# Kernel optimization log

Measured on AMD Instinct MI355X. Metric: run time of the kernel, lower is better.

## Reference

```python
import jax, jax.numpy as jnp
import numpy as np

B, D, H = 64, 2048, 2048


def setup_inputs() -> dict:
    key = jax.random.key(0)
    ks = jax.random.split(key, 10)
    s = 1.0 / np.sqrt(D)  # Linear init scale
    # small z scale keeps exp() gates in a sane range
    return {
        "t": jnp.zeros((), jnp.float32),
        "z": jax.random.normal(ks[0], (B, D), jnp.float32) * 0.02,
        "K": jax.random.normal(ks[1], (B, D), jnp.float32) * 0.02,
        "V": jax.random.normal(ks[2], (B, D, D), jnp.float32) * 0.02,
        "Wq": jax.random.normal(ks[3], (D, D), jnp.float32) * s,
        "bq": jnp.zeros((D,), jnp.float32),
        "Wk": jax.random.normal(ks[4], (D, D), jnp.float32) * s,
        "bk": jnp.zeros((D,), jnp.float32),
        "Wv": jax.random.normal(ks[5], (D, D), jnp.float32) * s,
        "bv": jnp.zeros((D,), jnp.float32),
        "W1": jax.random.normal(ks[6], (D, H), jnp.float32) * s,
        "b1": jnp.zeros((H,), jnp.float32),
        "W2": jax.random.normal(ks[7], (H, D), jnp.float32) * (1.0 / np.sqrt(H)),
        "b2": jnp.zeros((D,), jnp.float32),
    }


def reference(t, z, K, V, Wq, bq, Wk, bk, Wv, bv, W1, b1, W2, b2):
    # get_ode_gradient_nn: 2-layer tanh MLP (stand-in for user ode_func_net)
    dz = jnp.tanh(z @ W1 + b1) @ W2 + b2                 # [B, D]
    dK = jnp.exp(z @ Wk + bk)                            # exp gate, [B, D]
    v = z @ Wv + bv                                      # [B, D]
    dV = jnp.einsum("bd,be->bde", v, dK)                # rank-1 outer update, [B, D, D]
    q = jnp.exp(z @ Wq + bq)                             # [B, D]
    a = jnp.sum(q * dK, axis=-1, keepdims=True)          # q . dK, [B, 1]
    dq = q * (dz @ Wq + bq)                              # [B, D]
    da = a + jnp.sum(dq * K, axis=-1, keepdims=True)     # [B, 1]
    dc = jnp.einsum("bde,be->bd", dV, q) + jnp.einsum("bde,be->bd", V, dq)  # [B, D]
    return (dz, da, dc, dK, dV)
```

## Files before the change

### kernel.cpp

```cpp
#include <hip/hip_runtime.h>
#include <cstddef>
#include <math.h>

#define BB 64
#define DD 2048
#define HH 2048
#define BD (BB*DD)
#define WN (2048*2048)

typedef unsigned short u16;
typedef __attribute__((ext_vector_type(8))) short bf16x8;
typedef __attribute__((ext_vector_type(4))) float f32x4;
typedef __attribute__((ext_vector_type(4))) float f4;

__device__ __forceinline__ u16 f2b(float x) {
    union { float f; unsigned u; } v; v.f = x;
    unsigned r = v.u + 0x7FFFu + ((v.u >> 16) & 1u);
    return (u16)(r >> 16);
}

__device__ __forceinline__ void gload16(const void* g, void* l) {
    __builtin_amdgcn_global_load_lds(
        (__attribute__((address_space(1))) void*)g,
        (__attribute__((address_space(3))) void*)l, 16, 0, 0);
}


__device__ __forceinline__ void wconv_tile(
    u16* sm, const float* __restrict__ W, u16* __restrict__ T,
    int kb, int nb)
{
    int t = threadIdx.x;
    int k0 = kb * 64, n0 = nb * 64;
    {
        int r = t >> 2, c0 = (t & 3) * 16;
        const float* src = W + (size_t)(k0 + r) * DD + n0 + c0;
#pragma unroll
        for (int q = 0; q < 4; ++q) {
            float4 f = *(const float4*)(src + q * 4);
            sm[r * 66 + c0 + q*4 + 0] = f2b(f.x);
            sm[r * 66 + c0 + q*4 + 1] = f2b(f.y);
            sm[r * 66 + c0 + q*4 + 2] = f2b(f.z);
            sm[r * 66 + c0 + q*4 + 3] = f2b(f.w);
        }
    }
    __syncthreads();
    {
        int rn = t >> 2, ck = (t & 3) * 16;
        u16 o[16];
#pragma unroll
        for (int j = 0; j < 16; ++j) o[j] = sm[(ck + j) * 66 + rn];
        u16* dst = T + (size_t)(n0 + rn) * DD + k0 + ck;
        *(bf16x8*)dst       = *(bf16x8*)&o[0];
        *(bf16x8*)(dst + 8) = *(bf16x8*)&o[8];
    }
}

__device__ __forceinline__ void gemm_bf16_body(
    u16* sm, const u16* __restrict__ A, const u16* __restrict__ Wt,
    float* __restrict__ P, int kc, int nblk, int kblk)
{
    u16* Als = sm;
    u16* Wls = sm + 2048;
    const int t = threadIdx.x, w = t >> 6, lane = t & 63;
    const int n0 = nblk * 64;
    const int k0 = kblk * kc;

    f32x4 acc[4];
#pragma unroll
    for (int mt = 0; mt < 4; ++mt) acc[mt] = (f32x4){0.f, 0.f, 0.f, 0.f};

    const int srow = lane >> 2;
    const int sk   = (lane & 3) * 8;
    const u16* gA = A  + (size_t)(w * 16 + srow) * DD + k0 + sk;
    const u16* gW = Wt + (size_t)(n0 + w * 16 + srow) * DD + k0 + sk;
    u16* lA = &Als[w * 512];
    u16* lW = &Wls[w * 512];

    const int lane15 = lane & 15;
    const int k8 = (lane >> 4) * 8;

    for (int kk = 0; kk < kc; kk += 32) {
        gload16(gA, lA);
        gload16(gW, lW);
        gA += 32; gW += 32;
        __syncthreads();

        bf16x8 bfrag = *(const bf16x8*)&Wls[(w * 16 + lane15) * 32 + k8];
#pragma unroll
        for (int mt = 0; mt < 4; ++mt) {
            bf16x8 afrag = *(const bf16x8*)&Als[(mt * 16 + lane15) * 32 + k8];
            acc[mt] = __builtin_amdgcn_mfma_f32_16x16x32_bf16(
                afrag, bfrag, acc[mt], 0, 0, 0);
        }
        __syncthreads();
    }

    const int col = n0 + w * 16 + lane15;
    const int r4 = (lane >> 4) * 4;
#pragma unroll
    for (int mt = 0; mt < 4; ++mt)
#pragma unroll
        for (int j = 0; j < 4; ++j)
            P[(size_t)(mt * 16 + r4 + j) * DD + col] = acc[mt][j];
}

__device__ __forceinline__ void dv_body(
    const float* __restrict__ v, const float* __restrict__ dK,
    float* __restrict__ dV, int b, int chunk)
{
    int wave = threadIdx.x >> 6;
    int lane = threadIdx.x & 63;

    const f4* dK4 = (const f4*)(dK + ((size_t)b << 11));
    f4 dKr[8];
#pragma unroll
    for (int u = 0; u < 8; ++u) dKr[u] = dK4[u * 64 + lane];

    int row0 = chunk * 64 + wave * 16;
    for (int rr = 0; rr < 16; ++rr) {
        int row = row0 + rr;
        float vr = v[((size_t)b << 11) + row];
        f4* dV4 = (f4*)(dV + (((size_t)((b << 11) | row)) << 11));
#pragma unroll
        for (int u = 0; u < 8; ++u) {
            f4 o = vr * dKr[u];
            __builtin_nontemporal_store(o, &dV4[u * 64 + lane]);
        }
    }
}


__global__ __launch_bounds__(256) void wconv1(
    const float* __restrict__ W1, const float* __restrict__ Wk,
    const float* __restrict__ Wv, u16* __restrict__ W1t,
    u16* __restrict__ Wkt, u16* __restrict__ Wvt,
    const float* __restrict__ z, u16* __restrict__ zb)
{
    __shared__ u16 sm[64 * 66];
    int t = threadIdx.x;
    if (blockIdx.z == 3) {
        if (blockIdx.y != 0 || blockIdx.x >= 32) return;
        int i0 = blockIdx.x * 4096 + t * 16;
        u16 o[16];
#pragma unroll
        for (int q = 0; q < 4; ++q) {
            float4 f = *(const float4*)&z[i0 + q * 4];
            o[q*4+0] = f2b(f.x); o[q*4+1] = f2b(f.y);
            o[q*4+2] = f2b(f.z); o[q*4+3] = f2b(f.w);
        }
        *(bf16x8*)&zb[i0]     = *(bf16x8*)&o[0];
        *(bf16x8*)&zb[i0 + 8] = *(bf16x8*)&o[8];
        return;
    }
    const float* W = (blockIdx.z == 0) ? W1 : (blockIdx.z == 1) ? Wk : Wv;
    u16* T = (blockIdx.z == 0) ? W1t : (blockIdx.z == 1) ? Wkt : Wvt;
    wconv_tile(sm, W, T, blockIdx.x, blockIdx.y);
}

__global__ __launch_bounds__(256) void mA(
    const u16* __restrict__ zb, const u16* __restrict__ W1t,
    const u16* __restrict__ Wkt, const u16* __restrict__ Wvt,
    float* __restrict__ ph, float* __restrict__ pk, float* __restrict__ pv,
    const float* __restrict__ W2, const float* __restrict__ Wq,
    u16* __restrict__ W2t, u16* __restrict__ Wqt, int kc, int nG)
{
    __shared__ u16 sm[64 * 66];
    int blk = blockIdx.x;
    if (blk < 3 * nG) {
        int sel = blk / nG;
        int r   = blk - sel * nG;
        const u16* Wt = (sel == 0) ? W1t : (sel == 1) ? Wkt : Wvt;
        float* pool   = (sel == 0) ? ph  : (sel == 1) ? pk  : pv;
        int nblk = r & 31, kblk = r >> 5;
        gemm_bf16_body(sm, zb, Wt, pool + (size_t)kblk * 64 * DD,
                       kc, nblk, kblk);
    } else {
        int r = blk - 3 * nG;
        const float* W = (r < 1024) ? W2 : Wq;
        u16* T         = (r < 1024) ? W2t : Wqt;
        int rr = r & 1023;
        wconv_tile(sm, W, T, rr & 31, rr >> 5);
    }
}

__global__ __launch_bounds__(256) void mEp(
    const float* __restrict__ ph, const float* __restrict__ pk,
    const float* __restrict__ pv, const float* __restrict__ b1,
    const float* __restrict__ bk, const float* __restrict__ bv,
    u16* __restrict__ hb, float* __restrict__ dKo, float* __restrict__ vo,
    int KS)
{
    int blk = blockIdx.x;
    if (blk < 512) {
        int i = blk * 256 + threadIdx.x;
        float s = b1[i & (DD - 1)];
        for (int ks = 0; ks < KS; ++ks) s += ph[(size_t)ks * BD + i];
        hb[i] = f2b(tanhf(s));
    } else {
        int i = (blk - 512) * 256 + threadIdx.x;
        int d = i & (DD - 1);
        float sk = 0.f, sv = 0.f;
        for (int ks = 0; ks < KS; ++ks) {
            sk += pk[(size_t)ks * BD + i];
            sv += pv[(size_t)ks * BD + i];
        }
        dKo[i] = expf(sk + bk[d]);
        vo[i]  = sv + bv[d];
    }
}

__global__ __launch_bounds__(256) void mDZ(
    const float* __restrict__ v, const float* __restrict__ dK,
    float* __restrict__ dV, const u16* __restrict__ hb,
    const u16* __restrict__ W2t, float* __restrict__ p0, int kc, int nG)
{
    __shared__ u16 sm[4096];
    int blk = blockIdx.x;
    if (blk < 1024) {
        dv_body(v, dK, dV, blk >> 5, blk & 31);
    } else {
        int r = blk - 1024;
        int nblk = r & 31, kblk = r >> 5;
        gemm_bf16_body(sm, hb, W2t, p0 + (size_t)kblk * 64 * DD,
                       kc, nblk, kblk);
    }
}

__global__ __launch_bounds__(256) void ep_dz(
    const float* __restrict__ p, const float* __restrict__ b2,
    float* __restrict__ dz, u16* __restrict__ dzb, int KS)
{
    int i = blockIdx.x * 256 + threadIdx.x;
    float s = b2[i & (DD - 1)];
    for (int ks = 0; ks < KS; ++ks) s += p[(size_t)ks * BD + i];
    dz[i]  = s;
    dzb[i] = f2b(s);
}

__global__ __launch_bounds__(256) void mQ(
    const float* __restrict__ v, const float* __restrict__ dK,
    float* __restrict__ dV, const u16* __restrict__ zb,
    const u16* __restrict__ dzb, const u16* __restrict__ Wqt,
    float* __restrict__ pq, int kc, int nG)
{
    __shared__ u16 sm[4096];
    int blk = blockIdx.x;
    if (blk < 1024) {
        dv_body(v, dK, dV, 32 + (blk >> 5), blk & 31);
    } else {
        int r = blk - 1024;
        int zsel = (r >= nG) ? 1 : 0;
        int rr = r - zsel * nG;
        int nblk = rr & 31, kblk = rr >> 5;
        const u16* A = zsel ? dzb : zb;
        gemm_bf16_body(sm, A, Wqt,
                       pq + ((size_t)kblk * 128 + zsel * 64) * DD,
                       kc, nblk, kblk);
    }
}

__global__ __launch_bounds__(256) void ep_q_dq(
    const float* __restrict__ pq, const float* __restrict__ bq,
    float* __restrict__ qo, float* __restrict__ dqo, int KS)
{
    int i = blockIdx.x * 256 + threadIdx.x;
    int b = i >> 11, d = i & (DD - 1);
    float sq = 0.f, sd = 0.f;
    for (int ks = 0; ks < KS; ++ks) {
        const float* P = pq + (size_t)ks * (128 * DD);
        sq += P[(size_t)b * DD + d];
        sd += P[(size_t)(b + 64) * DD + d];
    }
    float bb = bq[d];
    float qv = expf(sq + bb);
    qo[i]  = qv;
    dqo[i] = qv * (sd + bb);
}

template<int MT>
__device__ __forceinline__ void gemm_body_f32(
    const float* __restrict__ A0, const float* __restrict__ A1,
    const float* __restrict__ W, float* __restrict__ part, int kc)
{
    constexpr int KC = 32;
    constexpr int RT = MT / 16;
    __shared__ float As[KC][MT];
    __shared__ float Ws[KC][64];

    const int t  = threadIdx.x;
    const int n0 = blockIdx.x * 64;
    const int k0 = blockIdx.y * kc;
    const int i  = t >> 4;
    const int j  = t & 15;

    float acc[RT][4];
#pragma unroll
    for (int r = 0; r < RT; ++r)
#pragma unroll
        for (int c = 0; c < 4; ++c) acc[r][c] = 0.f;

    for (int kk0 = 0; kk0 < kc; kk0 += KC) {
        {
            int kk = t >> 3;
            int nn = (t & 7) << 3;
            const float* s = W + (size_t)(k0 + kk0 + kk) * DD + n0 + nn;
            *(float4*)&Ws[kk][nn]     = *(const float4*)s;
            *(float4*)&Ws[kk][nn + 4] = *(const float4*)(s + 4);
        }
        if constexpr (MT == 64) {
            int m  = t & 63;
            int kb = (t >> 6) << 3;
            const float* s = A0 + (size_t)m * DD + k0 + kk0 + kb;
            float4 a0 = *(const float4*)s;
            float4 a1 = *(const float4*)(s + 4);
            As[kb+0][m] = a0.x; As[kb+1][m] = a0.y;
            As[kb+2][m] = a0.z; As[kb+3][m] = a0.w;
            As[kb+4][m] = a1.x; As[kb+5][m] = a1.y;
            As[kb+6][m] = a1.z; As[kb+7][m] = a1.w;
        } else {
            int m  = t & 127;
            int kb = (t >> 7) << 4;
            const float* base = (m < 64) ? (A0 + (size_t)m * DD)
                                         : (A1 + (size_t)(m - 64) * DD);
            const float* s = base + k0 + kk0 + kb;
#pragma unroll
            for (int p = 0; p < 4; ++p) {
                float4 av = *(const float4*)(s + p * 4);
                As[kb+p*4+0][m] = av.x; As[kb+p*4+1][m] = av.y;
                As[kb+p*4+2][m] = av.z; As[kb+p*4+3][m] = av.w;
            }
        }
        __syncthreads();
#pragma unroll
        for (int kk = 0; kk < KC; ++kk) {
            float4 wv = *(float4*)&Ws[kk][j << 2];
#pragma unroll
            for (int rq = 0; rq < RT / 4; ++rq) {
                float4 av = *(float4*)&As[kk][i * RT + rq * 4];
                acc[rq*4+0][0] = fmaf(av.x, wv.x, acc[rq*4+0][0]);
                acc[rq*4+0][1] = fmaf(av.x, wv.y, acc[rq*4+0][1]);
                acc[rq*4+0][2] = fmaf(av.x, wv.z, acc[rq*4+0][2]);
                acc[rq*4+0][3] = fmaf(av.x, wv.w, acc[rq*4+0][3]);
                acc[rq*4+1][0] = fmaf(av.y, wv.x, acc[rq*4+1][0]);
                acc[rq*4+1][1] = fmaf(av.y, wv.y, acc[rq*4+1][1]);
                acc[rq*4+1][2] = fmaf(av.y, wv.z, acc[rq*4+1][2]);
                acc[rq*4+1][3] = fmaf(av.y, wv.w, acc[rq*4+1][3]);
                acc[rq*4+2][0] = fmaf(av.z, wv.x, acc[rq*4+2][0]);
                acc[rq*4+2][1] = fmaf(av.z, wv.y, acc[rq*4+2][1]);
                acc[rq*4+2][2] = fmaf(av.z, wv.z, acc[rq*4+2][2]);
                acc[rq*4+2][3] = fmaf(av.z, wv.w, acc[rq*4+2][3]);
                acc[rq*4+3][0] = fmaf(av.w, wv.x, acc[rq*4+3][0]);
                acc[rq*4+3][1] = fmaf(av.w, wv.y, acc[rq*4+3][1]);
                acc[rq*4+3][2] = fmaf(av.w, wv.z, acc[rq*4+3][2]);
                acc[rq*4+3][3] = fmaf(av.w, wv.w, acc[rq*4+3][3]);
            }
        }
        __syncthreads();
    }

    float* P = part + (size_t)blockIdx.y * MT * DD + n0 + (j << 2);
#pragma unroll
    for (int r = 0; r < RT; ++r)
        *(float4*)&P[(size_t)(i * RT + r) * DD] =
            make_float4(acc[r][0], acc[r][1], acc[r][2], acc[r][3]);
}

__global__ __launch_bounds__(256) void gemm64(
    const float* __restrict__ A, const float* __restrict__ W,
    float* __restrict__ part, int kc)
{ gemm_body_f32<64>(A, A, W, part, kc); }

__global__ __launch_bounds__(256) void gemm64_z2(
    const float* __restrict__ A,
    const float* __restrict__ W0, const float* __restrict__ W1,
    float* __restrict__ p0, float* __restrict__ p1, int kc)
{
    const float* W = blockIdx.z ? W1 : W0;
    float*       P = blockIdx.z ? p1 : p0;
    gemm_body_f32<64>(A, A, W, P, kc);
}

__global__ __launch_bounds__(256) void gemm128(
    const float* __restrict__ A0, const float* __restrict__ A1,
    const float* __restrict__ W, float* __restrict__ part, int kc)
{ gemm_body_f32<128>(A0, A1, W, part, kc); }

__global__ __launch_bounds__(256) void epilogue_f32(
    const float* __restrict__ part, const float* __restrict__ bias,
    float* __restrict__ out, int act, int KS)
{
    int i = blockIdx.x * 256 + threadIdx.x;
    float s = bias[i & (DD - 1)];
    for (int ks = 0; ks < KS; ++ks) s += part[(size_t)ks * BD + i];
    if (act == 1) s = tanhf(s);
    out[i] = s;
}

__global__ __launch_bounds__(256) void ep_kv_f32(
    const float* __restrict__ pk, const float* __restrict__ pv,
    const float* __restrict__ bk, const float* __restrict__ bv,
    float* __restrict__ dKo, float* __restrict__ vo, int KS)
{
    int i = blockIdx.x * 256 + threadIdx.x;
    int d = i & (DD - 1);
    float sk = 0.f, sv = 0.f;
    for (int ks = 0; ks < KS; ++ks) {
        sk += pk[(size_t)ks * BD + i];
        sv += pv[(size_t)ks * BD + i];
    }
    dKo[i] = expf(sk + bk[d]);
    vo[i]  = sv + bv[d];
}

__global__ __launch_bounds__(256) void dv_write_full(
    const float* __restrict__ v, const float* __restrict__ dK,
    float* __restrict__ dV)
{
    dv_body(v, dK, dV, blockIdx.x >> 5, blockIdx.x & 31);
}

__global__ __launch_bounds__(256) void reduce_a_da(
    const float* __restrict__ q, const float* __restrict__ dK,
    const float* __restrict__ dq, const float* __restrict__ Kin,
    float* __restrict__ a_ws, float* __restrict__ da_out)
{
    int b = blockIdx.x;
    int t = threadIdx.x;
    const float* qb  = q   + (size_t)b * DD;
    const float* dKb = dK  + (size_t)b * DD;
    const float* dqb = dq  + (size_t)b * DD;
    const float* Kb  = Kin + (size_t)b * DD;

    float s1 = 0.f, s2 = 0.f;
    for (int i = t; i < DD; i += 256) {
        s1 = fmaf(qb[i],  dKb[i], s1);
        s2 = fmaf(dqb[i], Kb[i],  s2);
    }
#pragma unroll
    for (int off = 32; off; off >>= 1) {
        s1 += __shfl_down(s1, off);
        s2 += __shfl_down(s2, off);
    }
    __shared__ float r1[4], r2[4];
    if ((t & 63) == 0) { r1[t >> 6] = s1; r2[t >> 6] = s2; }
    __syncthreads();
    if (t == 0) {
        float a  = r1[0] + r1[1] + r1[2] + r1[3];
        float k2 = r2[0] + r2[1] + r2[2] + r2[3];
        a_ws[b]   = a;
        da_out[b] = a + k2;
    }
}

__global__ __launch_bounds__(256) void dc_dot(
    const float* __restrict__ V, const float* __restrict__ v,
    const float* __restrict__ dq, const float* __restrict__ a,
    float* __restrict__ dc)
{
    int b     = blockIdx.x >> 5;
    int chunk = blockIdx.x & 31;
    int wave  = threadIdx.x >> 6;
    int lane  = threadIdx.x & 63;

    const f4* dq4 = (const f4*)(dq + ((size_t)b << 11));
    f4 dqr[8];
#pragma unroll
    for (int u = 0; u < 8; ++u) dqr[u] = dq4[u * 64 + lane];
    float ab = a[b];

    int row0 = chunk * 64 + wave * 16;
    for (int g = 0; g < 4; ++g) {
        float dot[4];
#pragma unroll
        for (int r2 = 0; r2 < 4; ++r2) {
            int row = row0 + g * 4 + r2;
            const f4* V4 = (const f4*)(V + (((size_t)((b << 11) | row)) << 11));
            float d = 0.f;
#pragma unroll
            for (int u = 0; u < 8; ++u) {
                f4 Vv = __builtin_nontemporal_load(&V4[u * 64 + lane]);
                d += Vv[0] * dqr[u][0] + Vv[1] * dqr[u][1]
                   + Vv[2] * dqr[u][2] + Vv[3] * dqr[u][3];
            }
            dot[r2] = d;
        }
#pragma unroll
        for (int r2 = 0; r2 < 4; ++r2) {
            float d = dot[r2];
#pragma unroll
            for (int s = 32; s; s >>= 1) d += __shfl_down(d, s);
            if (lane == 0) {
                int row = row0 + g * 4 + r2;
                dc[((size_t)b << 11) + row] =
                    v[((size_t)b << 11) + row] * ab + d;
            }
        }
    }
}

extern "C" void kernel_launch(void* const* d_in, const int* in_sizes, int n_in,
                              void* d_out, int out_size, void* d_ws, size_t ws_size,
                              hipStream_t stream)
{
    const float* z   = (const float*)d_in[1];
    const float* Kin = (const float*)d_in[2];
    const float* Vin = (const float*)d_in[3];
    const float* Wq  = (const float*)d_in[4];
    const float* bq  = (const float*)d_in[5];
    const float* Wk  = (const float*)d_in[6];
    const float* bk  = (const float*)d_in[7];
    const float* Wv  = (const float*)d_in[8];
    const float* bv  = (const float*)d_in[9];
    const float* W1  = (const float*)d_in[10];
    const float* b1  = (const float*)d_in[11];
    const float* W2  = (const float*)d_in[12];
    const float* b2  = (const float*)d_in[13];

    float* out   = (float*)d_out;
    float* o_dz  = out;
    float* o_da  = out + BD;
    float* o_dc  = out + BD + BB;
    float* o_dK  = out + 2 * BD + BB;
    float* o_dV  = out + 3 * BD + BB;

    float* ws    = (float*)d_ws;
    float* ws_v  = ws;
    float* ws_q  = ws + BD;
    float* ws_dq = ws + 2 * BD;
    float* ws_a  = ws + 3 * BD;
    float* ws_h  = ws + 3 * BD + 64;
    u16*   zb    = (u16*)(ws + 4 * BD + 64);
    u16*   hb    = zb + BD;
    u16*   dzb   = hb + BD;
    u16*   wt    = dzb + BD;
    float* poolb = (float*)(wt + 5ull * WN);

    const size_t pre_fl = 4ull * BD + 64 + (3ull * BD + 5ull * WN) / 2;

    int KS = 0;
    for (int ks = 16; ks >= 4; ks >>= 1)
        if ((pre_fl + 3ull * ks * BD) * 4ull <= ws_size) { KS = ks; break; }

    dim3 blk(256);
    dim3 gE(BD / 256);

    if (KS) {
        int kc = DD / KS;
        int nG = 32 * KS;
        float* ph = poolb;
        float* pk = poolb + (size_t)KS * BD;
        float* pv = poolb + 2ull * KS * BD;
        float* p0 = poolb;
        float* pq = poolb;

        u16* W1t = wt;
        u16* W2t = wt + 1ull * WN;
        u16* Wkt = wt + 2ull * WN;
        u16* Wvt = wt + 3ull * WN;
        u16* Wqt = wt + 4ull * WN;

        wconv1<<<dim3(32, 32, 4), blk, 0, stream>>>(
            W1, Wk, Wv, W1t, Wkt, Wvt, z, zb);

        mA<<<dim3(3 * nG + 2048), blk, 0, stream>>>(
            zb, W1t, Wkt, Wvt, ph, pk, pv, W2, Wq, W2t, Wqt, kc, nG);

        mEp<<<dim3(1024), blk, 0, stream>>>(
            ph, pk, pv, b1, bk, bv, hb, o_dK, ws_v, KS);

        mDZ<<<dim3(1024 + nG), blk, 0, stream>>>(
            ws_v, o_dK, o_dV, hb, W2t, p0, kc, nG);

        ep_dz<<<gE, blk, 0, stream>>>(p0, b2, o_dz, dzb, KS);

        mQ<<<dim3(1024 + 2 * nG), blk, 0, stream>>>(
            ws_v, o_dK, o_dV, zb, dzb, Wqt, pq, kc, nG);

        ep_q_dq<<<gE, blk, 0, stream>>>(pq, bq, ws_q, ws_dq, KS);
    } else {
        float* pool = ws + 4 * BD + 64;
        int KSf = 16;
        while (KSf > 1 &&
               ((size_t)(4 * BD + 64) + 2ull * KSf * BD) * 4ull > ws_size)
            KSf >>= 1;
        int kc = DD / KSf;
        float* p0 = pool;
        float* p1 = pool + (size_t)KSf * BD;

        dim3 gG(DD / 64, KSf);
        dim3 gG2(DD / 64, KSf, 2);

        gemm64<<<gG, blk, 0, stream>>>(z, W1, p0, kc);
        epilogue_f32<<<gE, blk, 0, stream>>>(p0, b1, ws_h, 1, KSf);

        gemm64<<<gG, blk, 0, stream>>>(ws_h, W2, p0, kc);
        epilogue_f32<<<gE, blk, 0, stream>>>(p0, b2, o_dz, 0, KSf);

        gemm64_z2<<<gG2, blk, 0, stream>>>(z, Wk, Wv, p0, p1, kc);
        ep_kv_f32<<<gE, blk, 0, stream>>>(p0, p1, bk, bv, o_dK, ws_v, KSf);

        dv_write_full<<<dim3(BB * 32), blk, 0, stream>>>(ws_v, o_dK, o_dV);

        gemm128<<<gG, blk, 0, stream>>>(z, o_dz, Wq, p0, kc);
        ep_q_dq<<<gE, blk, 0, stream>>>(p0, bq, ws_q, ws_dq, KSf);
    }

    reduce_a_da<<<dim3(BB), blk, 0, stream>>>(ws_q, o_dK, ws_dq, Kin, ws_a, o_da);

    dc_dot<<<dim3(BB * 32), blk, 0, stream>>>(Vin, ws_v, ws_dq, ws_a, o_dc);
}
```

Before: 425.6 us.

## Replace split-K GEMMs with full-K pipelined GEMMs and fused epilogues

The split-K bf16 GEMMs that wrote partial sums to a pool are replaced by full-K GEMMs, one 64-column block each. These use a triple-buffered async LDS load pipeline and apply bias, tanh or exp in registers. This removes the separate reduction/epilogue kernels and the partial-sum memory traffic. It also folds the a/da reduction into the dc kernel, which drops several launches. The trade-off is that each GEMM now runs only 32 to 96 blocks over the full K range, so there is much less parallelism on the GEMM side, partly hidden by co-scheduling them with the dV writes.

```diff
diff --git a/kernel.cpp b/kernel.cpp
--- a/kernel.cpp
+++ b/kernel.cpp
@@ -56,53 +56,66 @@
     }
 }
 
-__device__ __forceinline__ void gemm_bf16_body(
-    u16* sm, const u16* __restrict__ A, const u16* __restrict__ Wt,
-    float* __restrict__ P, int kc, int nblk, int kblk)
-{
-    u16* Als = sm;
-    u16* Wls = sm + 2048;
+template<int NS>
+__device__ __forceinline__ void gemm_fullk(
+    u16* sm, const u16* __restrict__ A0, const u16* __restrict__ A1,
+    const u16* __restrict__ Wt, int nblk, f32x4* acc0, f32x4* acc1)
+{
+    constexpr int NS1 = NS + 1;
+    constexpr int REG = NS1 * 2048;
     const int t = threadIdx.x, w = t >> 6, lane = t & 63;
     const int n0 = nblk * 64;
-    const int k0 = kblk * kc;
-
-    f32x4 acc[4];
-#pragma unroll
-    for (int mt = 0; mt < 4; ++mt) acc[mt] = (f32x4){0.f, 0.f, 0.f, 0.f};
-
     const int srow = lane >> 2;
     const int sk   = (lane & 3) * 8;
-    const u16* gA = A  + (size_t)(w * 16 + srow) * DD + k0 + sk;
-    const u16* gW = Wt + (size_t)(n0 + w * 16 + srow) * DD + k0 + sk;
-    u16* lA = &Als[w * 512];
-    u16* lW = &Wls[w * 512];
+
+    const u16* gA0 = A0 + (size_t)(w * 16 + srow) * DD + sk;
+    const u16* gA1 = (NS == 2) ? A1 + (size_t)(w * 16 + srow) * DD + sk : A0;
+    const u16* gW  = Wt + (size_t)(n0 + w * 16 + srow) * DD + sk;
+    const int woff = w * 512;
 
     const int lane15 = lane & 15;
     const int k8 = (lane >> 4) * 8;
 
-    for (int kk = 0; kk < kc; kk += 32) {
-        gload16(gA, lA);
-        gload16(gW, lW);
-        gA += 32; gW += 32;
-        __syncthreads();
-
-        bf16x8 bfrag = *(const bf16x8*)&Wls[(w * 16 + lane15) * 32 + k8];
+    auto stage = [&](int it, int buf) {
+        u16* base = sm + buf * REG;
+        gload16(gA0 + it * 32, base + woff);
+        if constexpr (NS == 2) gload16(gA1 + it * 32, base + 2048 + woff);
+        gload16(gW + it * 32, base + (NS1 - 1) * 2048 + woff);
+    };
+
+    constexpr int nt = DD / 32;
+    stage(0, 0);
+    stage(1, 1);
+    for (int it = 0; it < nt; ++it) {
+        const int cur = it % 3;
+        if (it + 2 < nt) {
+            stage(it + 2, (it + 2) % 3);
+            if constexpr (NS == 1) asm volatile("s_waitcnt vmcnt(4)" ::: "memory");
+            else                   asm volatile("s_waitcnt vmcnt(6)" ::: "memory");
+        } else if (it + 1 < nt) {
+            if constexpr (NS == 1) asm volatile("s_waitcnt vmcnt(2)" ::: "memory");
+            else                   asm volatile("s_waitcnt vmcnt(3)" ::: "memory");
+        } else {
+            asm volatile("s_waitcnt vmcnt(0)" ::: "memory");
+        }
+        __builtin_amdgcn_s_barrier();
+
+        const u16* base = sm + cur * REG;
+        bf16x8 bfrag = *(const bf16x8*)&base[(NS1-1)*2048 + (w*16 + lane15)*32 + k8];
 #pragma unroll
         for (int mt = 0; mt < 4; ++mt) {
-            bf16x8 afrag = *(const bf16x8*)&Als[(mt * 16 + lane15) * 32 + k8];
-            acc[mt] = __builtin_amdgcn_mfma_f32_16x16x32_bf16(
-                afrag, bfrag, acc[mt], 0, 0, 0);
-        }
-        __syncthreads();
-    }
-
-    const int col = n0 + w * 16 + lane15;
-    const int r4 = (lane >> 4) * 4;
-#pragma unroll
-    for (int mt = 0; mt < 4; ++mt)
-#pragma unroll
-        for (int j = 0; j < 4; ++j)
-            P[(size_t)(mt * 16 + r4 + j) * DD + col] = acc[mt][j];
+            bf16x8 a0 = *(const bf16x8*)&base[(mt*16 + lane15)*32 + k8];
+            acc0[mt] = __builtin_amdgcn_mfma_f32_16x16x32_bf16(a0, bfrag, acc0[mt], 0, 0, 0);
+        }
+        if constexpr (NS == 2) {
+#pragma unroll
+            for (int mt = 0; mt < 4; ++mt) {
+                bf16x8 a1 = *(const bf16x8*)&base[2048 + (mt*16 + lane15)*32 + k8];
+                acc1[mt] = __builtin_amdgcn_mfma_f32_16x16x32_bf16(a1, bfrag, acc1[mt], 0, 0, 0);
+            }
+        }
+        __builtin_amdgcn_s_barrier();
+    }
 }
 
 __device__ __forceinline__ void dv_body(
@@ -161,22 +174,53 @@
 __global__ __launch_bounds__(256) void mA(
     const u16* __restrict__ zb, const u16* __restrict__ W1t,
     const u16* __restrict__ Wkt, const u16* __restrict__ Wvt,
-    float* __restrict__ ph, float* __restrict__ pk, float* __restrict__ pv,
+    const float* __restrict__ b1, const float* __restrict__ bk,
+    const float* __restrict__ bv, u16* __restrict__ hb,
+    float* __restrict__ dKo, float* __restrict__ vo,
     const float* __restrict__ W2, const float* __restrict__ Wq,
-    u16* __restrict__ W2t, u16* __restrict__ Wqt, int kc, int nG)
-{
-    __shared__ u16 sm[64 * 66];
+    u16* __restrict__ W2t, u16* __restrict__ Wqt)
+{
+    __shared__ u16 sm[3 * 4096];
     int blk = blockIdx.x;
-    if (blk < 3 * nG) {
-        int sel = blk / nG;
-        int r   = blk - sel * nG;
+    if (blk < 96) {
+        int sel  = blk >> 5;
+        int nblk = blk & 31;
         const u16* Wt = (sel == 0) ? W1t : (sel == 1) ? Wkt : Wvt;
-        float* pool   = (sel == 0) ? ph  : (sel == 1) ? pk  : pv;
-        int nblk = r & 31, kblk = r >> 5;
-        gemm_bf16_body(sm, zb, Wt, pool + (size_t)kblk * 64 * DD,
-                       kc, nblk, kblk);
+        f32x4 acc[4];
+#pragma unroll
+        for (int mt = 0; mt < 4; ++mt) acc[mt] = (f32x4){0.f,0.f,0.f,0.f};
+        gemm_fullk<1>(sm, zb, zb, Wt, nblk, acc, nullptr);
+
+        int w = threadIdx.x >> 6, lane = threadIdx.x & 63;
+        int col = nblk * 64 + w * 16 + (lane & 15);
+        int r4  = (lane >> 4) * 4;
+        if (sel == 0) {
+            float bb = b1[col];
+#pragma unroll
+            for (int mt = 0; mt < 4; ++mt)
+#pragma unroll
+                for (int j = 0; j < 4; ++j)
+                    hb[(size_t)(mt*16 + r4 + j) * DD + col] =
+                        f2b(tanhf(acc[mt][j] + bb));
+        } else if (sel == 1) {
+            float bb = bk[col];
+#pragma unroll
+            for (int mt = 0; mt < 4; ++mt)
+#pragma unroll
+                for (int j = 0; j < 4; ++j)
+                    dKo[(size_t)(mt*16 + r4 + j) * DD + col] =
+                        expf(acc[mt][j] + bb);
+        } else {
+            float bb = bv[col];
+#pragma unroll
+            for (int mt = 0; mt < 4; ++mt)
+#pragma unroll
+                for (int j = 0; j < 4; ++j)
+                    vo[(size_t)(mt*16 + r4 + j) * DD + col] =
+                        acc[mt][j] + bb;
+        }
     } else {
-        int r = blk - 3 * nG;
+        int r = blk - 96;
         const float* W = (r < 1024) ? W2 : Wq;
         u16* T         = (r < 1024) ? W2t : Wqt;
         int rr = r & 1023;
@@ -184,98 +228,147 @@
     }
 }
 
-__global__ __launch_bounds__(256) void mEp(
-    const float* __restrict__ ph, const float* __restrict__ pk,
-    const float* __restrict__ pv, const float* __restrict__ b1,
-    const float* __restrict__ bk, const float* __restrict__ bv,
-    u16* __restrict__ hb, float* __restrict__ dKo, float* __restrict__ vo,
-    int KS)
-{
+__global__ __launch_bounds__(256) void mDZ(
+    const u16* __restrict__ hb, const u16* __restrict__ W2t,
+    const float* __restrict__ b2, float* __restrict__ dz,
+    u16* __restrict__ dzb,
+    const float* __restrict__ v, const float* __restrict__ dK,
+    float* __restrict__ dV)
+{
+    __shared__ u16 sm[3 * 4096];
     int blk = blockIdx.x;
-    if (blk < 512) {
-        int i = blk * 256 + threadIdx.x;
-        float s = b1[i & (DD - 1)];
-        for (int ks = 0; ks < KS; ++ks) s += ph[(size_t)ks * BD + i];
-        hb[i] = f2b(tanhf(s));
+    if (blk < 32) {
+        f32x4 acc[4];
+#pragma unroll
+        for (int mt = 0; mt < 4; ++mt) acc[mt] = (f32x4){0.f,0.f,0.f,0.f};
+        gemm_fullk<1>(sm, hb, hb, W2t, blk, acc, nullptr);
+
+        int w = threadIdx.x >> 6, lane = threadIdx.x & 63;
+        int col = blk * 64 + w * 16 + (lane & 15);
+        int r4  = (lane >> 4) * 4;
+        float bb = b2[col];
+#pragma unroll
+        for (int mt = 0; mt < 4; ++mt)
+#pragma unroll
+            for (int j = 0; j < 4; ++j) {
+                float s = acc[mt][j] + bb;
+                size_t idx = (size_t)(mt*16 + r4 + j) * DD + col;
+                dz[idx]  = s;
+                dzb[idx] = f2b(s);
+            }
     } else {
-        int i = (blk - 512) * 256 + threadIdx.x;
-        int d = i & (DD - 1);
-        float sk = 0.f, sv = 0.f;
-        for (int ks = 0; ks < KS; ++ks) {
-            sk += pk[(size_t)ks * BD + i];
-            sv += pv[(size_t)ks * BD + i];
-        }
-        dKo[i] = expf(sk + bk[d]);
-        vo[i]  = sv + bv[d];
-    }
-}
-
-__global__ __launch_bounds__(256) void mDZ(
+        int r = blk - 32;
+        dv_body(v, dK, dV, r >> 5, r & 31);
+    }
+}
+
+__global__ __launch_bounds__(256) void mQ(
+    const u16* __restrict__ zb, const u16* __restrict__ dzb,
+    const u16* __restrict__ Wqt, const float* __restrict__ bq,
+    float* __restrict__ qo, float* __restrict__ dqo,
     const float* __restrict__ v, const float* __restrict__ dK,
-    float* __restrict__ dV, const u16* __restrict__ hb,
-    const u16* __restrict__ W2t, float* __restrict__ p0, int kc, int nG)
-{
-    __shared__ u16 sm[4096];
+    float* __restrict__ dV)
+{
+    __shared__ u16 sm[3 * 6144];
     int blk = blockIdx.x;
-    if (blk < 1024) {
-        dv_body(v, dK, dV, blk >> 5, blk & 31);
+    if (blk < 32) {
+        f32x4 az[4], ad[4];
+#pragma unroll
+        for (int mt = 0; mt < 4; ++mt) {
+            az[mt] = (f32x4){0.f,0.f,0.f,0.f};
+            ad[mt] = (f32x4){0.f,0.f,0.f,0.f};
+        }
+        gemm_fullk<2>(sm, zb, dzb, Wqt, blk, az, ad);
+
+        int w = threadIdx.x >> 6, lane = threadIdx.x & 63;
+        int col = blk * 64 + w * 16 + (lane & 15);
+        int r4  = (lane >> 4) * 4;
+        float bb = bq[col];
+#pragma unroll
+        for (int mt = 0; mt < 4; ++mt)
+#pragma unroll
+            for (int j = 0; j < 4; ++j) {
+                float qv = expf(az[mt][j] + bb);
+                size_t idx = (size_t)(mt*16 + r4 + j) * DD + col;
+                qo[idx]  = qv;
+                dqo[idx] = qv * (ad[mt][j] + bb);
+            }
     } else {
-        int r = blk - 1024;
-        int nblk = r & 31, kblk = r >> 5;
-        gemm_bf16_body(sm, hb, W2t, p0 + (size_t)kblk * 64 * DD,
-                       kc, nblk, kblk);
-    }
-}
-
-__global__ __launch_bounds__(256) void ep_dz(
-    const float* __restrict__ p, const float* __restrict__ b2,
-    float* __restrict__ dz, u16* __restrict__ dzb, int KS)
-{
-    int i = blockIdx.x * 256 + threadIdx.x;
-    float s = b2[i & (DD - 1)];
-    for (int ks = 0; ks < KS; ++ks) s += p[(size_t)ks * BD + i];
-    dz[i]  = s;
-    dzb[i] = f2b(s);
-}
-
-__global__ __launch_bounds__(256) void mQ(
-    const float* __restrict__ v, const float* __restrict__ dK,
-    float* __restrict__ dV, const u16* __restrict__ zb,
-    const u16* __restrict__ dzb, const u16* __restrict__ Wqt,
-    float* __restrict__ pq, int kc, int nG)
-{
-    __shared__ u16 sm[4096];
-    int blk = blockIdx.x;
-    if (blk < 1024) {
-        dv_body(v, dK, dV, 32 + (blk >> 5), blk & 31);
-    } else {
-        int r = blk - 1024;
-        int zsel = (r >= nG) ? 1 : 0;
-        int rr = r - zsel * nG;
-        int nblk = rr & 31, kblk = rr >> 5;
-        const u16* A = zsel ? dzb : zb;
-        gemm_bf16_body(sm, A, Wqt,
-                       pq + ((size_t)kblk * 128 + zsel * 64) * DD,
-                       kc, nblk, kblk);
-    }
-}
-
-__global__ __launch_bounds__(256) void ep_q_dq(
-    const float* __restrict__ pq, const float* __restrict__ bq,
-    float* __restrict__ qo, float* __restrict__ dqo, int KS)
-{
-    int i = blockIdx.x * 256 + threadIdx.x;
-    int b = i >> 11, d = i & (DD - 1);
-    float sq = 0.f, sd = 0.f;
-    for (int ks = 0; ks < KS; ++ks) {
-        const float* P = pq + (size_t)ks * (128 * DD);
-        sq += P[(size_t)b * DD + d];
-        sd += P[(size_t)(b + 64) * DD + d];
-    }
-    float bb = bq[d];
-    float qv = expf(sq + bb);
-    qo[i]  = qv;
-    dqo[i] = qv * (sd + bb);
+        int r = blk - 32;
+        dv_body(v, dK, dV, 32 + (r >> 5), r & 31);
+    }
+}
+
+__global__ __launch_bounds__(256) void dc_fin(
+    const float* __restrict__ V, const float* __restrict__ v,
+    const float* __restrict__ q, const float* __restrict__ dK,
+    const float* __restrict__ dq, const float* __restrict__ Kin,
+    float* __restrict__ da, float* __restrict__ dc)
+{
+    int b     = blockIdx.x >> 5;
+    int chunk = blockIdx.x & 31;
+    int t     = threadIdx.x;
+    int wave  = t >> 6, lane = t & 63;
+
+    const float* qb  = q   + (size_t)b * DD;
+    const float* dKb = dK  + (size_t)b * DD;
+    const float* dqb = dq  + (size_t)b * DD;
+    const float* Kb  = Kin + (size_t)b * DD;
+
+    float s1 = 0.f, s2 = 0.f;
+    for (int i = t; i < DD; i += 256) {
+        s1 = fmaf(qb[i],  dKb[i], s1);
+        s2 = fmaf(dqb[i], Kb[i],  s2);
+    }
+#pragma unroll
+    for (int off = 32; off; off >>= 1) {
+        s1 += __shfl_down(s1, off);
+        s2 += __shfl_down(s2, off);
+    }
+    __shared__ float r1[4], r2[4], sa;
+    if ((t & 63) == 0) { r1[t >> 6] = s1; r2[t >> 6] = s2; }
+    __syncthreads();
+    if (t == 0) {
+        float a = r1[0] + r1[1] + r1[2] + r1[3];
+        sa = a;
+        if (chunk == 0) da[b] = a + r2[0] + r2[1] + r2[2] + r2[3];
+    }
+    __syncthreads();
+    float ab = sa;
+
+    const f4* dq4 = (const f4*)(dq + ((size_t)b << 11));
+    f4 dqr[8];
+#pragma unroll
+    for (int u = 0; u < 8; ++u) dqr[u] = dq4[u * 64 + lane];
+
+    int row0 = chunk * 64 + wave * 16;
+    for (int g = 0; g < 4; ++g) {
+        float dot[4];
+#pragma unroll
+        for (int r2i = 0; r2i < 4; ++r2i) {
+            int row = row0 + g * 4 + r2i;
+            const f4* V4 = (const f4*)(V + (((size_t)((b << 11) | row)) << 11));
+            float d = 0.f;
+#pragma unroll
+            for (int u = 0; u < 8; ++u) {
+                f4 Vv = __builtin_nontemporal_load(&V4[u * 64 + lane]);
+                d += Vv[0] * dqr[u][0] + Vv[1] * dqr[u][1]
+                   + Vv[2] * dqr[u][2] + Vv[3] * dqr[u][3];
+            }
+            dot[r2i] = d;
+        }
+#pragma unroll
+        for (int r2i = 0; r2i < 4; ++r2i) {
+            float d = dot[r2i];
+#pragma unroll
+            for (int s = 32; s; s >>= 1) d += __shfl_down(d, s);
+            if (lane == 0) {
+                int row = row0 + g * 4 + r2i;
+                dc[((size_t)b << 11) + row] =
+                    v[((size_t)b << 11) + row] * ab + d;
+            }
+        }
+    }
 }
 
 template<int MT>
@@ -413,90 +506,29 @@
     vo[i]  = sv + bv[d];
 }
 
+__global__ __launch_bounds__(256) void ep_q_dq_f32(
+    const float* __restrict__ pq, const float* __restrict__ bq,
+    float* __restrict__ qo, float* __restrict__ dqo, int KS)
+{
+    int i = blockIdx.x * 256 + threadIdx.x;
+    int b = i >> 11, d = i & (DD - 1);
+    float sq = 0.f, sd = 0.f;
+    for (int ks = 0; ks < KS; ++ks) {
+        const float* P = pq + (size_t)ks * (128 * DD);
+        sq += P[(size_t)b * DD + d];
+        sd += P[(size_t)(b + 64) * DD + d];
+    }
+    float bb = bq[d];
+    float qv = expf(sq + bb);
+    qo[i]  = qv;
+    dqo[i] = qv * (sd + bb);
+}
+
 __global__ __launch_bounds__(256) void dv_write_full(
     const float* __restrict__ v, const float* __restrict__ dK,
     float* __restrict__ dV)
 {
     dv_body(v, dK, dV, blockIdx.x >> 5, blockIdx.x & 31);
-}
-
-__global__ __launch_bounds__(256) void reduce_a_da(
-    const float* __restrict__ q, const float* __restrict__ dK,
-    const float* __restrict__ dq, const float* __restrict__ Kin,
-    float* __restrict__ a_ws, float* __restrict__ da_out)
-{
-    int b = blockIdx.x;
-    int t = threadIdx.x;
-    const float* qb  = q   + (size_t)b * DD;
-    const float* dKb = dK  + (size_t)b * DD;
-    const float* dqb = dq  + (size_t)b * DD;
-    const float* Kb  = Kin + (size_t)b * DD;
-
-    float s1 = 0.f, s2 = 0.f;
-    for (int i = t; i < DD; i += 256) {
-        s1 = fmaf(qb[i],  dKb[i], s1);
-        s2 = fmaf(dqb[i], Kb[i],  s2);
-    }
-#pragma unroll
-    for (int off = 32; off; off >>= 1) {
-        s1 += __shfl_down(s1, off);
-        s2 += __shfl_down(s2, off);
-    }
-    __shared__ float r1[4], r2[4];
-    if ((t & 63) == 0) { r1[t >> 6] = s1; r2[t >> 6] = s2; }
-    __syncthreads();
-    if (t == 0) {
-        float a  = r1[0] + r1[1] + r1[2] + r1[3];
-        float k2 = r2[0] + r2[1] + r2[2] + r2[3];
-        a_ws[b]   = a;
-        da_out[b] = a + k2;
-    }
-}
-
-__global__ __launch_bounds__(256) void dc_dot(
-    const float* __restrict__ V, const float* __restrict__ v,
-    const float* __restrict__ dq, const float* __restrict__ a,
-    float* __restrict__ dc)
-{
-    int b     = blockIdx.x >> 5;
-    int chunk = blockIdx.x & 31;
-    int wave  = threadIdx.x >> 6;
-    int lane  = threadIdx.x & 63;
-
-    const f4* dq4 = (const f4*)(dq + ((size_t)b << 11));
-    f4 dqr[8];
-#pragma unroll
-    for (int u = 0; u < 8; ++u) dqr[u] = dq4[u * 64 + lane];
-    float ab = a[b];
-
-    int row0 = chunk * 64 + wave * 16;
-    for (int g = 0; g < 4; ++g) {
-        float dot[4];
-#pragma unroll
-        for (int r2 = 0; r2 < 4; ++r2) {
-            int row = row0 + g * 4 + r2;
-            const f4* V4 = (const f4*)(V + (((size_t)((b << 11) | row)) << 11));
-            float d = 0.f;
-#pragma unroll
-            for (int u = 0; u < 8; ++u) {
-                f4 Vv = __builtin_nontemporal_load(&V4[u * 64 + lane]);
-                d += Vv[0] * dqr[u][0] + Vv[1] * dqr[u][1]
-                   + Vv[2] * dqr[u][2] + Vv[3] * dqr[u][3];
-            }
-            dot[r2] = d;
-        }
-#pragma unroll
-        for (int r2 = 0; r2 < 4; ++r2) {
-            float d = dot[r2];
-#pragma unroll
-            for (int s = 32; s; s >>= 1) d += __shfl_down(d, s);
-            if (lane == 0) {
-                int row = row0 + g * 4 + r2;
-                dc[((size_t)b << 11) + row] =
-                    v[((size_t)b << 11) + row] * ab + d;
-            }
-        }
-    }
 }
 
 extern "C" void kernel_launch(void* const* d_in, const int* in_sizes, int n_in,
@@ -528,32 +560,17 @@
     float* ws_v  = ws;
     float* ws_q  = ws + BD;
     float* ws_dq = ws + 2 * BD;
-    float* ws_a  = ws + 3 * BD;
     float* ws_h  = ws + 3 * BD + 64;
     u16*   zb    = (u16*)(ws + 4 * BD + 64);
     u16*   hb    = zb + BD;
     u16*   dzb   = hb + BD;
     u16*   wt    = dzb + BD;
-    float* poolb = (float*)(wt + 5ull * WN);
 
     const size_t pre_fl = 4ull * BD + 64 + (3ull * BD + 5ull * WN) / 2;
 
-    int KS = 0;
-    for (int ks = 16; ks >= 4; ks >>= 1)
-        if ((pre_fl + 3ull * ks * BD) * 4ull <= ws_size) { KS = ks; break; }
-
     dim3 blk(256);
-    dim3 gE(BD / 256);
-
-    if (KS) {
-        int kc = DD / KS;
-        int nG = 32 * KS;
-        float* ph = poolb;
-        float* pk = poolb + (size_t)KS * BD;
-        float* pv = poolb + 2ull * KS * BD;
-        float* p0 = poolb;
-        float* pq = poolb;
-
+
+    if (pre_fl * 4ull <= ws_size) {
         u16* W1t = wt;
         u16* W2t = wt + 1ull * WN;
         u16* Wkt = wt + 2ull * WN;
@@ -563,21 +580,14 @@
         wconv1<<<dim3(32, 32, 4), blk, 0, stream>>>(
             W1, Wk, Wv, W1t, Wkt, Wvt, z, zb);
 
-        mA<<<dim3(3 * nG + 2048), blk, 0, stream>>>(
-            zb, W1t, Wkt, Wvt, ph, pk, pv, W2, Wq, W2t, Wqt, kc, nG);
-
-        mEp<<<dim3(1024), blk, 0, stream>>>(
-            ph, pk, pv, b1, bk, bv, hb, o_dK, ws_v, KS);
-
-        mDZ<<<dim3(1024 + nG), blk, 0, stream>>>(
-            ws_v, o_dK, o_dV, hb, W2t, p0, kc, nG);
-
-        ep_dz<<<gE, blk, 0, stream>>>(p0, b2, o_dz, dzb, KS);
-
-        mQ<<<dim3(1024 + 2 * nG), blk, 0, stream>>>(
-            ws_v, o_dK, o_dV, zb, dzb, Wqt, pq, kc, nG);
-
-        ep_q_dq<<<gE, blk, 0, stream>>>(pq, bq, ws_q, ws_dq, KS);
+        mA<<<dim3(96 + 2048), blk, 0, stream>>>(
+            zb, W1t, Wkt, Wvt, b1, bk, bv, hb, o_dK, ws_v, W2, Wq, W2t, Wqt);
+
+        mDZ<<<dim3(32 + 1024), blk, 0, stream>>>(
+            hb, W2t, b2, o_dz, dzb, ws_v, o_dK, o_dV);
+
+        mQ<<<dim3(32 + 1024), blk, 0, stream>>>(
+            zb, dzb, Wqt, bq, ws_q, ws_dq, ws_v, o_dK, o_dV);
     } else {
         float* pool = ws + 4 * BD + 64;
         int KSf = 16;
@@ -590,6 +600,7 @@
 
         dim3 gG(DD / 64, KSf);
         dim3 gG2(DD / 64, KSf, 2);
+        dim3 gE(BD / 256);
 
         gemm64<<<gG, blk, 0, stream>>>(z, W1, p0, kc);
         epilogue_f32<<<gE, blk, 0, stream>>>(p0, b1, ws_h, 1, KSf);
@@ -603,10 +614,9 @@
         dv_write_full<<<dim3(BB * 32), blk, 0, stream>>>(ws_v, o_dK, o_dV);
 
         gemm128<<<gG, blk, 0, stream>>>(z, o_dz, Wq, p0, kc);
-        ep_q_dq<<<gE, blk, 0, stream>>>(p0, bq, ws_q, ws_dq, KSf);
-    }
-
-    reduce_a_da<<<dim3(BB), blk, 0, stream>>>(ws_q, o_dK, ws_dq, Kin, ws_a, o_da);
-
-    dc_dot<<<dim3(BB * 32), blk, 0, stream>>>(Vin, ws_v, ws_dq, ws_a, o_dc);
-}
+        ep_q_dq_f32<<<gE, blk, 0, stream>>>(p0, bq, ws_q, ws_dq, KSf);
+    }
+
+    dc_fin<<<dim3(BB * 32), blk, 0, stream>>>(
+        Vin, ws_v, ws_q, o_dK, ws_dq, Kin, o_da, o_dc);
+}
```

Result: faster. 411.7 us (-3.3%).
